# Kernel tuning notes

Measured on AMD Instinct MI355X. Metric: run time of the kernel, lower is better.

## Reference

```python
import jax, jax.numpy as jnp
import numpy as np

B_SZ, SEQ, D_MODEL = 1, 2048, 1024
D_IN, N_STATE, DT_RANK, KSIZE = 2048, 16, 64, 3


def setup_inputs() -> dict:
    key = jax.random.key(0)
    ks = jax.random.split(key, 7)
    x = jax.random.normal(ks[0], (B_SZ, SEQ, D_MODEL), jnp.float32)
    W_in = jax.random.normal(ks[1], (D_MODEL, 2 * D_IN), jnp.float32) * 0.02
    conv_w = jax.random.normal(ks[2], (D_IN, 1, KSIZE), jnp.float32) * 0.1  # OIH, depthwise
    W_x = jax.random.normal(ks[3], (D_IN, DT_RANK + 2 * N_STATE), jnp.float32) * 0.02
    W_delta = jax.random.normal(ks[4], (DT_RANK, D_IN), jnp.float32) * 0.02
    b_delta = jnp.zeros((D_IN,), jnp.float32)
    # Keras initializer: A_log[d, n] = n+1 (arange 1..N repeated over d_in rows)
    A_log = jnp.tile(jnp.arange(1, N_STATE + 1, dtype=jnp.float32)[None, :], (D_IN, 1))
    D = jnp.ones((D_IN,), jnp.float32)
    W_out = jax.random.normal(ks[5], (D_IN, D_MODEL), jnp.float32) * 0.02
    return dict(x=x, W_in=W_in, conv_w=conv_w, W_x=W_x, W_delta=W_delta,
                b_delta=b_delta, A_log=A_log, D=D, W_out=W_out)


def selective_scan(u, delta, A, Bm, Cm, D):
    # u, delta: (b,l,d); A: (d,n); Bm, Cm: (b,l,n); D: (d,)
    dA = jnp.einsum('bld,dn->bldn', delta, A)
    dB_u = jnp.einsum('bld,bld,bln->bldn', delta, u, Bm)
    # shift dA left by one step, zero at the end (matches pad+slice in source)
    dA_shift = jnp.concatenate([dA[:, 1:], jnp.zeros_like(dA[:, :1])], axis=1)
    # reversed cumulative sum along time, then exp
    dA_cs = jnp.exp(jnp.flip(jnp.cumsum(jnp.flip(dA_shift, axis=1), axis=1), axis=1))
    xs = jnp.cumsum(dB_u * dA_cs, axis=1) / (dA_cs + 1e-12)
    y = jnp.einsum('bldn,bln->bld', xs, Cm)
    return y + u * D


def reference(x, W_in, conv_w, W_x, W_delta, b_delta, A_log, D, W_out):
    d_in = conv_w.shape[0]
    ksz = conv_w.shape[2]
    n = A_log.shape[1]
    dtr = W_delta.shape[0]
    x_and_res = x @ W_in                       # (b,l,2*d_in)
    xi, res = x_and_res[..., :d_in], x_and_res[..., d_in:]
    # depthwise causal conv over time (channels_first with left padding k-1)
    xc = jnp.transpose(xi, (0, 2, 1))          # (b,d_in,l)
    xc = jax.lax.conv_general_dilated(
        xc, conv_w, window_strides=(1,), padding=[(ksz - 1, 0)],
        dimension_numbers=('NCH', 'OIH', 'NCH'), feature_group_count=d_in)
    xi = jnp.transpose(xc, (0, 2, 1))          # (b,l,d_in)
    xi = xi * jax.nn.sigmoid(xi)               # swish
    # SSM
    A = -jnp.exp(A_log)
    x_dbl = xi @ W_x                           # (b,l,dtr+2n)
    delta_lr = x_dbl[..., :dtr]
    Bm = x_dbl[..., dtr:dtr + n]
    Cm = x_dbl[..., dtr + n:]
    delta = jax.nn.softplus(delta_lr @ W_delta + b_delta)
    y = selective_scan(xi, delta, A, Bm, Cm, D)
    y = y * (res * jax.nn.sigmoid(res))
    return y @ W_out
```

## Files before the change

### kernel.cpp

```cpp
#include <hip/hip_runtime.h>
#include <hip/hip_bf16.h>
#include <math.h>

#define SEQ     2048
#define D_MODEL 1024
#define D_IN    2048
#define N_STATE 16
#define DT_RANK 64
#define XDBL_W  96
#define XDBL_LD 128
#define LC      64
#define NCH     32
#define DT      32
#define WX_KSPLIT 16
#define WX_KSEG   (D_IN / WX_KSPLIT)
#define OUT_KSPLIT 4
#define OUT_KSEG   (D_IN / OUT_KSPLIT)

#define LOG2E   1.4426950408889634f

typedef __attribute__((ext_vector_type(8))) _Float16 f16x8;
typedef __attribute__((ext_vector_type(4))) float f32x4;

__device__ __forceinline__ float fast_exp2(float x) { return __builtin_amdgcn_exp2f(x); }
__device__ __forceinline__ float fast_rcp(float x)  { return __builtin_amdgcn_rcpf(x); }

__device__ __forceinline__ ushort f2h(float x) {
    _Float16 h = (_Float16)x;
    return __builtin_bit_cast(ushort, h);
}
__device__ __forceinline__ float h2f(ushort u) {
    return (float)__builtin_bit_cast(_Float16, u);
}

__device__ __forceinline__ void gload16(const ushort* g, ushort* l) {
    __builtin_amdgcn_global_load_lds(
        (const __attribute__((address_space(1))) void*)g,
        (__attribute__((address_space(3))) void*)l, 16, 0, 0);
}

#define GL_DEFS                                                                \
    const int lane8 = lane >> 3;                                               \
    const int scol  = (lane & 7) ^ lane8;                                      \
    const int wq    = wave * 8;

#define STAGE_GL(SRC, DST, BASE, LDK, KOFF)                                    \
    _Pragma("unroll")                                                          \
    for (int q = 0; q < 4; ++q) {                                              \
        const int rr = q * 32 + wq + lane8;                                    \
        gload16(&SRC[(size_t)((BASE) + rr) * (LDK) + (KOFF) + scol * 8],       \
                ((ushort*)DST) + (q * 256 + wave * 64) * 8);                   \
    }

#define COMPUTE_KS(KS)                                                         \
    {                                                                          \
        const int slot = ((((KS) << 2) | l4) ^ sw) * 8;                        \
        f16x8 ah[4], al[4], bb[4];                                             \
        _Pragma("unroll")                                                      \
        for (int f = 0; f < 4; ++f) {                                          \
            const int ar = mw + f * 16 + l15;                                  \
            const int br = nw + f * 16 + l15;                                  \
            ah[f] = *(const f16x8*)&lA[0][ar][slot];                           \
            al[f] = *(const f16x8*)&lA[1][ar][slot];                           \
            bb[f] = *(const f16x8*)&lB[br][slot];                              \
        }                                                                      \
        _Pragma("unroll")                                                      \
        for (int i = 0; i < 4; ++i)                                            \
            _Pragma("unroll")                                                  \
            for (int j = 0; j < 4; ++j) {                                      \
                acc[i][j] = __builtin_amdgcn_mfma_f32_16x16x32_f16(            \
                    ah[i], bb[j], acc[i][j], 0, 0, 0);                         \
                acc[i][j] = __builtin_amdgcn_mfma_f32_16x16x32_f16(            \
                    al[i], bb[j], acc[i][j], 0, 0, 0);                         \
            }                                                                  \
    }

template <int CTRL>
__device__ __forceinline__ float dpp_add(float x) {
    int y = __builtin_amdgcn_update_dpp(0, __float_as_int(x), CTRL, 0xF, 0xF, true);
    return x + __int_as_float(y);
}

__global__ __launch_bounds__(256) void split_f16(
    const float* __restrict__ in, ushort* __restrict__ hi,
    ushort* __restrict__ lo)
{
    const int i = blockIdx.x * 256 + threadIdx.x;
    const float4 v = *(const float4*)&in[(size_t)i * 4];
    ushort4 h, l;
    h.x = f2h(v.x); l.x = f2h(v.x - h2f(h.x));
    h.y = f2h(v.y); l.y = f2h(v.y - h2f(h.y));
    h.z = f2h(v.z); l.z = f2h(v.z - h2f(h.z));
    h.w = f2h(v.w); l.w = f2h(v.w - h2f(h.w));
    *(ushort4*)&hi[(size_t)i * 4] = h;
    *(ushort4*)&lo[(size_t)i * 4] = l;
}

__global__ __launch_bounds__(256) void trans_f16(
    const float* __restrict__ in, ushort* __restrict__ out, int R, int C)
{
    __shared__ float tile[32][33];
    const int c0 = blockIdx.x * 32;
    const int r0 = blockIdx.y * 32;
    const int tc = threadIdx.x & 31;
    const int tr = threadIdx.x >> 5;
#pragma unroll
    for (int q = 0; q < 4; ++q)
        tile[tr + 8 * q][tc] = in[(size_t)(r0 + tr + 8 * q) * C + c0 + tc];
    __syncthreads();
#pragma unroll
    for (int q = 0; q < 4; ++q)
        out[(size_t)(c0 + tr + 8 * q) * R + r0 + tc] = f2h(tile[tc][tr + 8 * q]);
}

__global__ __launch_bounds__(256) void trans_f16_pad(
    const float* __restrict__ in, ushort* __restrict__ out, int R, int Csrc)
{
    __shared__ float tile[32][33];
    const int c0 = blockIdx.x * 32;
    const int r0 = blockIdx.y * 32;
    const int tc = threadIdx.x & 31;
    const int tr = threadIdx.x >> 5;
#pragma unroll
    for (int q = 0; q < 4; ++q) {
        const int c = c0 + tc;
        tile[tr + 8 * q][tc] =
            (c < Csrc) ? in[(size_t)(r0 + tr + 8 * q) * Csrc + c] : 0.f;
    }
    __syncthreads();
#pragma unroll
    for (int q = 0; q < 4; ++q)
        out[(size_t)(c0 + tr + 8 * q) * R + r0 + tc] = f2h(tile[tc][tr + 8 * q]);
}

__global__ __launch_bounds__(256) void gemm_mfma3(
    const ushort* __restrict__ Ahi, const ushort* __restrict__ Alo,
    const ushort* __restrict__ Bf,
    float* __restrict__ C0, float* __restrict__ C1, int nsplit,
    int M, int N, int K, int ldc0, int ldc1)
{
    __shared__ ushort lA[2][128][64];
    __shared__ ushort lB[128][64];

    const int t    = threadIdx.x;
    const int m0   = blockIdx.y * 128;
    const int n0   = blockIdx.x * 128;
    const int wave = t >> 6;
    const int lane = t & 63;
    const int mw   = (wave & 1) * 64;
    const int nw   = (wave >> 1) * 64;
    const int l15  = lane & 15;
    const int l4   = lane >> 4;
    const int sw   = l15 & 7;
    GL_DEFS

    f32x4 acc[4][4];
#pragma unroll
    for (int i = 0; i < 4; ++i)
#pragma unroll
        for (int j = 0; j < 4; ++j)
            acc[i][j] = (f32x4){0.f, 0.f, 0.f, 0.f};

    for (int k0 = 0; k0 < K; k0 += 64) {
        __syncthreads();
        STAGE_GL(Ahi, lA[0], m0, K, k0)
        STAGE_GL(Alo, lA[1], m0, K, k0)
        STAGE_GL(Bf,  lB,    n0, K, k0)
        __syncthreads();
        COMPUTE_KS(0)
        COMPUTE_KS(1)
    }

#pragma unroll
    for (int i = 0; i < 4; ++i) {
        const int rowg = m0 + mw + i * 16 + l4 * 4;
#pragma unroll
        for (int j = 0; j < 4; ++j) {
            const int colg = n0 + nw + j * 16 + l15;
            if (colg < nsplit) {
#pragma unroll
                for (int v = 0; v < 4; ++v)
                    C0[(size_t)(rowg + v) * ldc0 + colg] = acc[i][j][v];
            } else {
                const int cc = colg - nsplit;
#pragma unroll
                for (int v = 0; v < 4; ++v) {
                    const float r = acc[i][j][v];
                    C1[(size_t)(rowg + v) * ldc1 + cc] =
                        r * fast_rcp(1.f + fast_exp2(-LOG2E * r));
                }
            }
        }
    }
}

__global__ __launch_bounds__(256) void gemm_wx_mfma(
    const ushort* __restrict__ Ahi, const ushort* __restrict__ Alo,
    const ushort* __restrict__ Bf, float* __restrict__ part)
{
    __shared__ ushort lA[2][128][64];
    __shared__ ushort lB[128][64];

    const int t    = threadIdx.x;
    const int kb   = blockIdx.x;
    const int m0   = blockIdx.y * 128;
    const int wave = t >> 6;
    const int lane = t & 63;
    const int mw   = (wave & 1) * 64;
    const int nw   = (wave >> 1) * 64;
    const int l15  = lane & 15;
    const int l4   = lane >> 4;
    const int sw   = l15 & 7;
    const int kbase = kb * WX_KSEG;
    GL_DEFS

    f32x4 acc[4][4];
#pragma unroll
    for (int i = 0; i < 4; ++i)
#pragma unroll
        for (int j = 0; j < 4; ++j)
            acc[i][j] = (f32x4){0.f, 0.f, 0.f, 0.f};

    for (int k0 = 0; k0 < WX_KSEG; k0 += 64) {
        __syncthreads();
        STAGE_GL(Ahi, lA[0], m0, D_IN, kbase + k0)
        STAGE_GL(Alo, lA[1], m0, D_IN, kbase + k0)
        STAGE_GL(Bf,  lB,    0,  D_IN, kbase + k0)
        __syncthreads();
        COMPUTE_KS(0)
        COMPUTE_KS(1)
    }

#pragma unroll
    for (int i = 0; i < 4; ++i) {
        const int rowg = m0 + mw + i * 16 + l4 * 4;
#pragma unroll
        for (int j = 0; j < 4; ++j) {
            const int colg = nw + j * 16 + l15;
#pragma unroll
            for (int v = 0; v < 4; ++v)
                part[((size_t)kb * SEQ + rowg + v) * XDBL_LD + colg] =
                    acc[i][j][v];
        }
    }
}

__global__ __launch_bounds__(256) void wx_reduce(
    const float* __restrict__ part, float* __restrict__ xdbl)
{
    const size_t i = (size_t)(blockIdx.x * 256 + threadIdx.x) * 4;
    float4 s = *(const float4*)&part[i];
#pragma unroll
    for (int kb = 1; kb < WX_KSPLIT; ++kb) {
        const float4 v = *(const float4*)&part[(size_t)kb * SEQ * XDBL_LD + i];
        s.x += v.x; s.y += v.y; s.z += v.z; s.w += v.w;
    }
    *(float4*)&xdbl[i] = s;
}

__global__ __launch_bounds__(256) void gemm_out_mfma(
    const ushort* __restrict__ Ahi, const ushort* __restrict__ Alo,
    const ushort* __restrict__ Bf,
    float* __restrict__ p01, float* __restrict__ p23)
{
    __shared__ ushort lA[2][128][64];
    __shared__ ushort lB[128][64];

    const int t    = threadIdx.x;
    const int n0   = blockIdx.x * 128;
    const int m0   = blockIdx.y * 128;
    const int kb   = blockIdx.z;
    const int wave = t >> 6;
    const int lane = t & 63;
    const int mw   = (wave & 1) * 64;
    const int nw   = (wave >> 1) * 64;
    const int l15  = lane & 15;
    const int l4   = lane >> 4;
    const int sw   = l15 & 7;
    const int kbase = kb * OUT_KSEG;
    GL_DEFS

    f32x4 acc[4][4];
#pragma unroll
    for (int i = 0; i < 4; ++i)
#pragma unroll
        for (int j = 0; j < 4; ++j)
            acc[i][j] = (f32x4){0.f, 0.f, 0.f, 0.f};

    for (int k0 = 0; k0 < OUT_KSEG; k0 += 64) {
        __syncthreads();
        STAGE_GL(Ahi, lA[0], m0, D_IN, kbase + k0)
        STAGE_GL(Alo, lA[1], m0, D_IN, kbase + k0)
        STAGE_GL(Bf,  lB,    n0, D_IN, kbase + k0)
        __syncthreads();
        COMPUTE_KS(0)
        COMPUTE_KS(1)
    }

    float* base = (kb & 2) ? p23 : p01;
    base += (size_t)(kb & 1) * SEQ * D_MODEL;
#pragma unroll
    for (int i = 0; i < 4; ++i) {
        const int rowg = m0 + mw + i * 16 + l4 * 4;
#pragma unroll
        for (int j = 0; j < 4; ++j) {
            const int colg = n0 + nw + j * 16 + l15;
#pragma unroll
            for (int v = 0; v < 4; ++v)
                base[(size_t)(rowg + v) * D_MODEL + colg] = acc[i][j][v];
        }
    }
}

__global__ __launch_bounds__(256) void out_reduce(
    const float* __restrict__ p01, const float* __restrict__ p23,
    float* __restrict__ out)
{
    const size_t i = (size_t)(blockIdx.x * 256 + threadIdx.x) * 4;
    const size_t MN = (size_t)SEQ * D_MODEL;
    const float4 a = *(const float4*)&p01[i];
    const float4 b = *(const float4*)&p01[i + MN];
    const float4 c = *(const float4*)&p23[i];
    const float4 d = *(const float4*)&p23[i + MN];
    float4 s;
    s.x = ((a.x + b.x) + c.x) + d.x;
    s.y = ((a.y + b.y) + c.y) + d.y;
    s.z = ((a.z + b.z) + c.z) + d.z;
    s.w = ((a.w + b.w) + c.w) + d.w;
    *(float4*)&out[i] = s;
}

__global__ __launch_bounds__(256) void gemm128(
    const float* __restrict__ A, const float* __restrict__ B,
    float* __restrict__ C, int M, int N, int K,
    int lda, int ldb, int ldc,
    const float* __restrict__ bias, int act)
{
    __shared__ float As[16][132];
    __shared__ float Bs[16][132];

    const int t   = threadIdx.x;
    const int bn0 = blockIdx.x * 128;
    const int bm0 = blockIdx.y * 128;
    const int tx  = t & 15;
    const int ty  = t >> 4;

    const int ar  = t >> 2;
    const int ak  = (t & 3) * 4;
    const int bk  = t >> 5;
    const int bn4 = (t & 31) * 4;

    float acc[8][8];
#pragma unroll
    for (int i = 0; i < 8; ++i)
#pragma unroll
        for (int j = 0; j < 8; ++j) acc[i][j] = 0.f;

    for (int k0 = 0; k0 < K; k0 += 16) {
        float4 a0 = *(const float4*)&A[(size_t)(bm0 + ar)      * lda + k0 + ak];
        float4 a1 = *(const float4*)&A[(size_t)(bm0 + ar + 64) * lda + k0 + ak];
        float4 b0 = *(const float4*)&B[(size_t)(k0 + bk)     * ldb + bn0 + bn4];
        float4 b1 = *(const float4*)&B[(size_t)(k0 + bk + 8) * ldb + bn0 + bn4];

        __syncthreads();
        As[ak + 0][ar] = a0.x; As[ak + 1][ar] = a0.y;
        As[ak + 2][ar] = a0.z; As[ak + 3][ar] = a0.w;
        As[ak + 0][ar + 64] = a1.x; As[ak + 1][ar + 64] = a1.y;
        As[ak + 2][ar + 64] = a1.z; As[ak + 3][ar + 64] = a1.w;
        *(float4*)&Bs[bk][bn4]     = b0;
        *(float4*)&Bs[bk + 8][bn4] = b1;
        __syncthreads();

#pragma unroll
        for (int kk = 0; kk < 16; ++kk) {
            float a[8], b[8];
            ((float4*)a)[0] = *(const float4*)&As[kk][ty * 8];
            ((float4*)a)[1] = *(const float4*)&As[kk][ty * 8 + 4];
            ((float4*)b)[0] = *(const float4*)&Bs[kk][tx * 8];
            ((float4*)b)[1] = *(const float4*)&Bs[kk][tx * 8 + 4];
#pragma unroll
            for (int i = 0; i < 8; ++i)
#pragma unroll
                for (int j = 0; j < 8; ++j)
                    acc[i][j] = fmaf(a[i], b[j], acc[i][j]);
        }
    }

    const int row = bm0 + ty * 8;
    const int col = bn0 + tx * 8;
#pragma unroll
    for (int i = 0; i < 8; ++i) {
        float vals[8];
#pragma unroll
        for (int j = 0; j < 8; ++j) {
            float v = acc[i][j];
            if (act == 1) {
                v += bias[col + j];
                v = (v > 20.f) ? v : log1pf(__expf(v));
            }
            vals[j] = v;
        }
        *(float4*)&C[(size_t)(row + i) * ldc + col]     = ((float4*)vals)[0];
        *(float4*)&C[(size_t)(row + i) * ldc + col + 4] = ((float4*)vals)[1];
    }
}

__global__ __launch_bounds__(256) void conv_silu_split(
    const float* __restrict__ xi, const float* __restrict__ cw,
    float* __restrict__ u, ushort* __restrict__ uhi, ushort* __restrict__ ulo)
{
    const int id = blockIdx.x * 256 + threadIdx.x;
    const int l = id >> 11;
    const int d = id & (D_IN - 1);
    const float w0 = cw[d * 3 + 0];
    const float w1 = cw[d * 3 + 1];
    const float w2 = cw[d * 3 + 2];
    const float x0  = xi[(size_t)l * D_IN + d];
    const float xm1 = (l >= 1) ? xi[(size_t)(l - 1) * D_IN + d] : 0.f;
    const float xm2 = (l >= 2) ? xi[(size_t)(l - 2) * D_IN + d] : 0.f;
    const float v = w0 * xm2 + w1 * xm1 + w2 * x0;
    const float s = fast_rcp(1.f + fast_exp2(-LOG2E * v));
    const float uu = v * s;
    u[id] = uu;
    const ushort h = f2h(uu);
    uhi[id] = h;
    ulo[id] = f2h(uu - h2f(h));
}

__global__ __launch_bounds__(256) void csum64(
    const float* __restrict__ delta, double* __restrict__ csum)
{
    const int d = blockIdx.x * 256 + threadIdx.x;
    const int c = blockIdx.y;
    double s = 0.0;
    for (int i = 0; i < LC; ++i)
        s += (double)delta[(size_t)(c * LC + i) * D_IN + d];
    csum[(size_t)c * D_IN + d] = s;
}

__global__ __launch_bounds__(256) void chunk_prefix(
    const double* __restrict__ csum, double* __restrict__ P0,
    double* __restrict__ Td)
{
    const int d = blockIdx.x * 256 + threadIdx.x;
    double P = 0.0;
    for (int c = 0; c < NCH; ++c) {
        P0[(size_t)c * D_IN + d] = P;
        P += csum[(size_t)c * D_IN + d];
    }
    Td[d] = P;
}

__global__ __launch_bounds__(256) void sfx_precompute(
    const float* __restrict__ delta, const double* __restrict__ P0,
    const double* __restrict__ Td, float* __restrict__ sfx)
{
    const int d = blockIdx.x * 256 + threadIdx.x;
    const int c = blockIdx.y;
    double P = P0[(size_t)c * D_IN + d];
    const double T = Td[d];
    for (int i = 0; i < LC; ++i) {
        const size_t row = (size_t)(c * LC + i) * D_IN + d;
        P += (double)delta[row];
        sfx[row] = (float)fmax(T - P, 0.0);
    }
}

__global__ __launch_bounds__(512) void scan_partA(
    const float* __restrict__ delta, const float* __restrict__ u,
    const float* __restrict__ sfxbuf, const float* __restrict__ xdbl,
    const float* __restrict__ Alog, float* __restrict__ Wc)
{
    __shared__ float2 spA[LC][DT];
    __shared__ float  sBA[LC][16];

    const int t  = threadIdx.x;
    const int c  = blockIdx.x;
    const int d0 = blockIdx.y * DT;

    {
        const int r = t >> 3, c4 = (t & 7) * 4;
        const size_t row = (size_t)(c * LC + r) * D_IN + d0 + c4;
        const float4 dv4 = *(const float4*)&delta[row];
        const float4 uv4 = *(const float4*)&u[row];
        const float4 sx4 = *(const float4*)&sfxbuf[row];
        spA[r][c4 + 0] = make_float2(dv4.x * uv4.x, sx4.x);
        spA[r][c4 + 1] = make_float2(dv4.y * uv4.y, sx4.y);
        spA[r][c4 + 2] = make_float2(dv4.z * uv4.z, sx4.z);
        spA[r][c4 + 3] = make_float2(dv4.w * uv4.w, sx4.w);
    }
    if (t < 256) {
        const int r = t >> 2, c4 = (t & 3) * 4;
        *(float4*)&sBA[r][c4] =
            *(const float4*)&xdbl[(size_t)(c * LC + r) * XDBL_LD + DT_RANK + c4];
    }
    __syncthreads();

    const int n  = t & 15;
    const int dq = t >> 4;
    const int d  = d0 + dq;
    const float An2 = -expf(Alog[d * N_STATE + n]) * LOG2E;

    float W = 0.f;
#pragma unroll
    for (int i = 0; i < LC; ++i) {
        const float2 p = spA[i][dq];
        W = fmaf(p.x * sBA[i][n], fast_exp2(An2 * p.y), W);
    }
    Wc[((size_t)c * D_IN + d) * N_STATE + n] = W;
}

__global__ __launch_bounds__(256) void scan_combine(float* __restrict__ Wc)
{
    const int id = blockIdx.x * 256 + threadIdx.x;
    float W = 0.f;
    for (int c = 0; c < NCH; ++c) {
        const size_t idx = (size_t)c * (D_IN * N_STATE) + id;
        const float w = Wc[idx];
        Wc[idx] = W;
        W += w;
    }
}

__global__ __launch_bounds__(512) void scan_partC(
    const float* __restrict__ delta, const float* __restrict__ u,
    const float* __restrict__ xdbl, const float* __restrict__ W0buf,
    const float* __restrict__ sfxbuf, const float* __restrict__ Alog,
    const float* __restrict__ Dvec, const float* __restrict__ rgbuf,
    float* __restrict__ yg)
{
    __shared__ float4 spack[LC][DT];
    __shared__ float2 sbc[LC][16];

    const int t  = threadIdx.x;
    const int c  = blockIdx.x;
    const int d0 = blockIdx.y * DT;

    {
        const int r = t >> 3, c4 = (t & 7) * 4;
        const size_t row = (size_t)(c * LC + r) * D_IN + d0 + c4;
        const float4 dv4 = *(const float4*)&delta[row];
        const float4 uv4 = *(const float4*)&u[row];
        const float4 sx4 = *(const float4*)&sfxbuf[row];
        const float4 rg4 = *(const float4*)&rgbuf[row];
        spack[r][c4 + 0] = make_float4(dv4.x * uv4.x, sx4.x, uv4.x, rg4.x);
        spack[r][c4 + 1] = make_float4(dv4.y * uv4.y, sx4.y, uv4.y, rg4.y);
        spack[r][c4 + 2] = make_float4(dv4.z * uv4.z, sx4.z, uv4.z, rg4.z);
        spack[r][c4 + 3] = make_float4(dv4.w * uv4.w, sx4.w, uv4.w, rg4.w);
    }
    if (t < 256) {
        const int r = t >> 2, n4 = (t & 3) * 4;
        const float4 b4 = *(const float4*)&xdbl[(size_t)(c * LC + r) * XDBL_LD + DT_RANK + n4];
        const float4 c4v = *(const float4*)&xdbl[(size_t)(c * LC + r) * XDBL_LD + DT_RANK + 16 + n4];
        sbc[r][n4 + 0] = make_float2(b4.x, c4v.x);
        sbc[r][n4 + 1] = make_float2(b4.y, c4v.y);
        sbc[r][n4 + 2] = make_float2(b4.z, c4v.z);
        sbc[r][n4 + 3] = make_float2(b4.w, c4v.w);
    }
    __syncthreads();

    const int n  = t & 15;
    const int dq = t >> 4;
    const int d  = d0 + dq;
    const float An2 = -expf(Alog[d * N_STATE + n]) * LOG2E;
    const float Dd = Dvec[d];

    float W = W0buf[((size_t)c * D_IN + d) * N_STATE + n];

#pragma unroll
    for (int i = 0; i < LC; ++i) {
        const float4 p = spack[i][dq];
        const float2 bc = sbc[i][n];
        const float E = fast_exp2(An2 * p.y);
        W = fmaf(p.x * bc.x, E, W);
        const float xs = W * fast_rcp(E + 1e-12f);
        float contrib = xs * bc.y;
        contrib = dpp_add<0xB1>(contrib);
        contrib = dpp_add<0x4E>(contrib);
        contrib = dpp_add<0x128>(contrib);
        contrib = dpp_add<0x124>(contrib);
        if (n == 0) {
            yg[(size_t)(c * LC + i) * D_IN + d] =
                fmaf(p.z, Dd, contrib) * p.w;
        }
    }
}

extern "C" void kernel_launch(void* const* d_in, const int* in_sizes, int n_in,
                              void* d_out, int out_size, void* d_ws, size_t ws_size,
                              hipStream_t stream)
{
    const float* x      = (const float*)d_in[0];
    const float* W_in   = (const float*)d_in[1];
    const float* conv_w = (const float*)d_in[2];
    const float* W_x    = (const float*)d_in[3];
    const float* W_del  = (const float*)d_in[4];
    const float* b_del  = (const float*)d_in[5];
    const float* A_log  = (const float*)d_in[6];
    const float* Dv     = (const float*)d_in[7];
    const float* W_out  = (const float*)d_in[8];
    float* out = (float*)d_out;

    char* ws = (char*)d_ws;
    float*  xi    = (float*)(ws + 0);
    float*  wxp   = (float*)(ws + 0);
    float*  sfx   = (float*)(ws + 0);
    ushort* yg_hi = (ushort*)(ws + 0);
    ushort* yg_lo = (ushort*)(ws + 8388608);
    float*  rg    = (float*)(ws + 16777216);
    float*  p01   = (float*)(ws + 16777216);
    ushort* x_hi  = (ushort*)(ws + 33554432);
    ushort* x_lo  = (ushort*)(ws + 37748736);
    float*  u     = (float*)(ws + 33554432);
    ushort* wo    = (ushort*)(ws + 33554432);
    float*  xdbl  = (float*)(ws + 50331648);
    ushort* wi    = (ushort*)(ws + 51380224);
    ushort* u_hi  = (ushort*)(ws + 51380224);
    ushort* u_lo  = (ushort*)(ws + 59768832);
    float*  delta = (float*)(ws + 51380224);
    float*  p23   = (float*)(ws + 51380224);
    float*  Wc    = (float*)(ws + 68157440);
    double* csum  = (double*)(ws + 72351744);
    double* P0    = (double*)(ws + 72876032);
    double* Td    = (double*)(ws + 73400320);
    ushort* wx    = (ushort*)(ws + 73416704);
    float*  yg    = delta;

    trans_f16<<<dim3(4096 / 32, 1024 / 32), 256, 0, stream>>>(
        W_in, wi, 1024, 4096);

    split_f16<<<(SEQ * D_MODEL / 4) / 256, 256, 0, stream>>>(x, x_hi, x_lo);

    gemm_mfma3<<<dim3(4096 / 128, 2048 / 128), 256, 0, stream>>>(
        x_hi, x_lo, wi, xi, rg, D_IN,
        SEQ, 2 * D_IN, D_MODEL, D_IN, D_IN);

    conv_silu_split<<<(SEQ * D_IN) / 256, 256, 0, stream>>>(
        xi, conv_w, u, u_hi, u_lo);

    trans_f16_pad<<<dim3(XDBL_LD / 32, D_IN / 32), 256, 0, stream>>>(
        W_x, wx, D_IN, XDBL_W);

    gemm_wx_mfma<<<dim3(WX_KSPLIT, SEQ / 128), 256, 0, stream>>>(
        u_hi, u_lo, wx, wxp);
    wx_reduce<<<(SEQ * XDBL_LD / 4) / 256, 256, 0, stream>>>(wxp, xdbl);

    gemm128<<<dim3(2048 / 128, 2048 / 128), 256, 0, stream>>>(
        xdbl, W_del, delta, SEQ, D_IN, DT_RANK, XDBL_LD, D_IN, D_IN,
        b_del, 1);

    csum64<<<dim3(D_IN / 256, NCH), 256, 0, stream>>>(delta, csum);
    chunk_prefix<<<D_IN / 256, 256, 0, stream>>>(csum, P0, Td);
    sfx_precompute<<<dim3(D_IN / 256, NCH), 256, 0, stream>>>(delta, P0, Td, sfx);

    scan_partA<<<dim3(NCH, D_IN / DT), 512, 0, stream>>>(
        delta, u, sfx, xdbl, A_log, Wc);
    scan_combine<<<(D_IN * N_STATE) / 256, 256, 0, stream>>>(Wc);
    scan_partC<<<dim3(NCH, D_IN / DT), 512, 0, stream>>>(
        delta, u, xdbl, Wc, sfx, A_log, Dv, rg, yg);

    split_f16<<<(SEQ * D_IN / 4) / 256, 256, 0, stream>>>(yg, yg_hi, yg_lo);

    trans_f16<<<dim3(1024 / 32, 2048 / 32), 256, 0, stream>>>(
        W_out, wo, 2048, 1024);

    gemm_out_mfma<<<dim3(D_MODEL / 128, SEQ / 128, OUT_KSPLIT), 256, 0, stream>>>(
        yg_hi, yg_lo, wo, p01, p23);
    out_reduce<<<(SEQ * D_MODEL / 4) / 256, 256, 0, stream>>>(p01, p23, out);
}
```

Before: 240.0 us.

## Fuse chunk delta sums into delta GEMM epilogue and halve scan threads

The softplus delta GEMM epilogue now computes per-64-row chunk column sums in double and writes them directly. This removes the separate csum64 and chunk_prefix kernels, and sfx_precompute derives its prefix and total from csum itself. The scan partA and partC kernels now use 256 threads, each handling two state indices, which halves block size and shortens the DPP reduction. The cost is extra double-precision work and shared memory in the GEMM epilogue, redundant prefix loops in every sfx block, and scalar rather than float4 loads in the scan kernels.

```diff
diff --git a/kernel.cpp b/kernel.cpp
--- a/kernel.cpp
+++ b/kernel.cpp
@@ -334,10 +334,11 @@
     const float* __restrict__ A, const float* __restrict__ B,
     float* __restrict__ C, int M, int N, int K,
     int lda, int ldb, int ldc,
-    const float* __restrict__ bias, int act)
+    const float* __restrict__ bias, double* __restrict__ csumOut)
 {
     __shared__ float As[16][132];
     __shared__ float Bs[16][132];
+    __shared__ double dpart[16][128];
 
     const int t   = threadIdx.x;
     const int bn0 = blockIdx.x * 128;
@@ -388,20 +389,33 @@
 
     const int row = bm0 + ty * 8;
     const int col = bn0 + tx * 8;
+    double dsum[8];
+#pragma unroll
+    for (int j = 0; j < 8; ++j) dsum[j] = 0.0;
 #pragma unroll
     for (int i = 0; i < 8; ++i) {
         float vals[8];
 #pragma unroll
         for (int j = 0; j < 8; ++j) {
-            float v = acc[i][j];
-            if (act == 1) {
-                v += bias[col + j];
-                v = (v > 20.f) ? v : log1pf(__expf(v));
-            }
+            float v = acc[i][j] + bias[col + j];
+            v = (v > 20.f) ? v : log1pf(__expf(v));
             vals[j] = v;
+            dsum[j] += (double)v;
         }
         *(float4*)&C[(size_t)(row + i) * ldc + col]     = ((float4*)vals)[0];
         *(float4*)&C[(size_t)(row + i) * ldc + col + 4] = ((float4*)vals)[1];
+    }
+
+#pragma unroll
+    for (int j = 0; j < 8; ++j) dpart[ty][tx * 8 + j] = dsum[j];
+    __syncthreads();
+    {
+        const int colr = t & 127;
+        const int half = t >> 7;
+        double s = 0.0;
+#pragma unroll
+        for (int q = 0; q < 8; ++q) s += dpart[half * 8 + q][colr];
+        csumOut[(size_t)((bm0 >> 6) + half) * D_IN + bn0 + colr] = s;
     }
 }
 
@@ -427,38 +441,18 @@
     ulo[id] = f2h(uu - h2f(h));
 }
 
-__global__ __launch_bounds__(256) void csum64(
-    const float* __restrict__ delta, double* __restrict__ csum)
+__global__ __launch_bounds__(256) void sfx_precompute(
+    const float* __restrict__ delta, const double* __restrict__ csum,
+    float* __restrict__ sfx)
 {
     const int d = blockIdx.x * 256 + threadIdx.x;
     const int c = blockIdx.y;
-    double s = 0.0;
-    for (int i = 0; i < LC; ++i)
-        s += (double)delta[(size_t)(c * LC + i) * D_IN + d];
-    csum[(size_t)c * D_IN + d] = s;
-}
-
-__global__ __launch_bounds__(256) void chunk_prefix(
-    const double* __restrict__ csum, double* __restrict__ P0,
-    double* __restrict__ Td)
-{
-    const int d = blockIdx.x * 256 + threadIdx.x;
-    double P = 0.0;
-    for (int c = 0; c < NCH; ++c) {
-        P0[(size_t)c * D_IN + d] = P;
-        P += csum[(size_t)c * D_IN + d];
-    }
-    Td[d] = P;
-}
-
-__global__ __launch_bounds__(256) void sfx_precompute(
-    const float* __restrict__ delta, const double* __restrict__ P0,
-    const double* __restrict__ Td, float* __restrict__ sfx)
-{
-    const int d = blockIdx.x * 256 + threadIdx.x;
-    const int c = blockIdx.y;
-    double P = P0[(size_t)c * D_IN + d];
-    const double T = Td[d];
+    double S = 0.0, P = 0.0;
+    for (int c2 = 0; c2 < NCH; ++c2) {
+        if (c2 == c) P = S;
+        S += csum[(size_t)c2 * D_IN + d];
+    }
+    const double T = S;
     for (int i = 0; i < LC; ++i) {
         const size_t row = (size_t)(c * LC + i) * D_IN + d;
         P += (double)delta[row];
@@ -466,48 +460,51 @@
     }
 }
 
-__global__ __launch_bounds__(512) void scan_partA(
+__global__ __launch_bounds__(256) void scan_partA(
     const float* __restrict__ delta, const float* __restrict__ u,
     const float* __restrict__ sfxbuf, const float* __restrict__ xdbl,
     const float* __restrict__ Alog, float* __restrict__ Wc)
 {
     __shared__ float2 spA[LC][DT];
-    __shared__ float  sBA[LC][16];
+    __shared__ float2 sbA[LC][8];
 
     const int t  = threadIdx.x;
     const int c  = blockIdx.x;
     const int d0 = blockIdx.y * DT;
 
-    {
-        const int r = t >> 3, c4 = (t & 7) * 4;
-        const size_t row = (size_t)(c * LC + r) * D_IN + d0 + c4;
-        const float4 dv4 = *(const float4*)&delta[row];
-        const float4 uv4 = *(const float4*)&u[row];
-        const float4 sx4 = *(const float4*)&sfxbuf[row];
-        spA[r][c4 + 0] = make_float2(dv4.x * uv4.x, sx4.x);
-        spA[r][c4 + 1] = make_float2(dv4.y * uv4.y, sx4.y);
-        spA[r][c4 + 2] = make_float2(dv4.z * uv4.z, sx4.z);
-        spA[r][c4 + 3] = make_float2(dv4.w * uv4.w, sx4.w);
-    }
-    if (t < 256) {
-        const int r = t >> 2, c4 = (t & 3) * 4;
-        *(float4*)&sBA[r][c4] =
-            *(const float4*)&xdbl[(size_t)(c * LC + r) * XDBL_LD + DT_RANK + c4];
+#pragma unroll
+    for (int q = 0; q < 8; ++q) {
+        const int e = q * 256 + t;
+        const int r = e >> 5, col = e & 31;
+        const size_t row = (size_t)(c * LC + r) * D_IN + d0 + col;
+        spA[r][col] = make_float2(delta[row] * u[row], sfxbuf[row]);
+    }
+#pragma unroll
+    for (int q = 0; q < 2; ++q) {
+        const int e = q * 256 + t;
+        const int r = e >> 3, n8e = e & 7;
+        const size_t base = (size_t)(c * LC + r) * XDBL_LD + DT_RANK;
+        sbA[r][n8e] = make_float2(xdbl[base + n8e], xdbl[base + 8 + n8e]);
     }
     __syncthreads();
 
-    const int n  = t & 15;
-    const int dq = t >> 4;
+    const int dq = t >> 3;
+    const int n8 = t & 7;
     const int d  = d0 + dq;
-    const float An2 = -expf(Alog[d * N_STATE + n]) * LOG2E;
-
-    float W = 0.f;
+    const float An2a = -expf(Alog[d * N_STATE + n8]) * LOG2E;
+    const float An2b = -expf(Alog[d * N_STATE + n8 + 8]) * LOG2E;
+
+    float W0 = 0.f, W1 = 0.f;
 #pragma unroll
     for (int i = 0; i < LC; ++i) {
         const float2 p = spA[i][dq];
-        W = fmaf(p.x * sBA[i][n], fast_exp2(An2 * p.y), W);
-    }
-    Wc[((size_t)c * D_IN + d) * N_STATE + n] = W;
+        const float2 b = sbA[i][n8];
+        W0 = fmaf(p.x * b.x, fast_exp2(An2a * p.y), W0);
+        W1 = fmaf(p.x * b.y, fast_exp2(An2b * p.y), W1);
+    }
+    const size_t o = ((size_t)c * D_IN + d) * N_STATE + n8;
+    Wc[o]     = W0;
+    Wc[o + 8] = W1;
 }
 
 __global__ __launch_bounds__(256) void scan_combine(float* __restrict__ Wc)
@@ -522,7 +519,7 @@
     }
 }
 
-__global__ __launch_bounds__(512) void scan_partC(
+__global__ __launch_bounds__(256) void scan_partC(
     const float* __restrict__ delta, const float* __restrict__ u,
     const float* __restrict__ xdbl, const float* __restrict__ W0buf,
     const float* __restrict__ sfxbuf, const float* __restrict__ Alog,
@@ -530,56 +527,57 @@
     float* __restrict__ yg)
 {
     __shared__ float4 spack[LC][DT];
-    __shared__ float2 sbc[LC][16];
+    __shared__ float4 sbc[LC][8];
 
     const int t  = threadIdx.x;
     const int c  = blockIdx.x;
     const int d0 = blockIdx.y * DT;
 
-    {
-        const int r = t >> 3, c4 = (t & 7) * 4;
-        const size_t row = (size_t)(c * LC + r) * D_IN + d0 + c4;
-        const float4 dv4 = *(const float4*)&delta[row];
-        const float4 uv4 = *(const float4*)&u[row];
-        const float4 sx4 = *(const float4*)&sfxbuf[row];
-        const float4 rg4 = *(const float4*)&rgbuf[row];
-        spack[r][c4 + 0] = make_float4(dv4.x * uv4.x, sx4.x, uv4.x, rg4.x);
-        spack[r][c4 + 1] = make_float4(dv4.y * uv4.y, sx4.y, uv4.y, rg4.y);
-        spack[r][c4 + 2] = make_float4(dv4.z * uv4.z, sx4.z, uv4.z, rg4.z);
-        spack[r][c4 + 3] = make_float4(dv4.w * uv4.w, sx4.w, uv4.w, rg4.w);
-    }
-    if (t < 256) {
-        const int r = t >> 2, n4 = (t & 3) * 4;
-        const float4 b4 = *(const float4*)&xdbl[(size_t)(c * LC + r) * XDBL_LD + DT_RANK + n4];
-        const float4 c4v = *(const float4*)&xdbl[(size_t)(c * LC + r) * XDBL_LD + DT_RANK + 16 + n4];
-        sbc[r][n4 + 0] = make_float2(b4.x, c4v.x);
-        sbc[r][n4 + 1] = make_float2(b4.y, c4v.y);
-        sbc[r][n4 + 2] = make_float2(b4.z, c4v.z);
-        sbc[r][n4 + 3] = make_float2(b4.w, c4v.w);
+#pragma unroll
+    for (int q = 0; q < 8; ++q) {
+        const int e = q * 256 + t;
+        const int r = e >> 5, col = e & 31;
+        const size_t row = (size_t)(c * LC + r) * D_IN + d0 + col;
+        const float dv = delta[row];
+        const float uv = u[row];
+        spack[r][col] = make_float4(dv * uv, sfxbuf[row], uv, rgbuf[row]);
+    }
+#pragma unroll
+    for (int q = 0; q < 2; ++q) {
+        const int e = q * 256 + t;
+        const int r = e >> 3, n8e = e & 7;
+        const size_t base = (size_t)(c * LC + r) * XDBL_LD + DT_RANK;
+        sbc[r][n8e] = make_float4(xdbl[base + n8e],      xdbl[base + 16 + n8e],
+                                  xdbl[base + 8 + n8e],  xdbl[base + 24 + n8e]);
     }
     __syncthreads();
 
-    const int n  = t & 15;
-    const int dq = t >> 4;
+    const int dq = t >> 3;
+    const int n8 = t & 7;
     const int d  = d0 + dq;
-    const float An2 = -expf(Alog[d * N_STATE + n]) * LOG2E;
+    const float An2a = -expf(Alog[d * N_STATE + n8]) * LOG2E;
+    const float An2b = -expf(Alog[d * N_STATE + n8 + 8]) * LOG2E;
     const float Dd = Dvec[d];
 
-    float W = W0buf[((size_t)c * D_IN + d) * N_STATE + n];
+    const size_t wo = ((size_t)c * D_IN + d) * N_STATE + n8;
+    float W0 = W0buf[wo];
+    float W1 = W0buf[wo + 8];
 
 #pragma unroll
     for (int i = 0; i < LC; ++i) {
-        const float4 p = spack[i][dq];
-        const float2 bc = sbc[i][n];
-        const float E = fast_exp2(An2 * p.y);
-        W = fmaf(p.x * bc.x, E, W);
-        const float xs = W * fast_rcp(E + 1e-12f);
-        float contrib = xs * bc.y;
+        const float4 p  = spack[i][dq];
+        const float4 bc = sbc[i][n8];
+        const float E0 = fast_exp2(An2a * p.y);
+        const float E1 = fast_exp2(An2b * p.y);
+        W0 = fmaf(p.x * bc.x, E0, W0);
+        W1 = fmaf(p.x * bc.z, E1, W1);
+        const float xs0 = W0 * fast_rcp(E0 + 1e-12f);
+        const float xs1 = W1 * fast_rcp(E1 + 1e-12f);
+        float contrib = fmaf(xs0, bc.y, xs1 * bc.w);
         contrib = dpp_add<0xB1>(contrib);
         contrib = dpp_add<0x4E>(contrib);
-        contrib = dpp_add<0x128>(contrib);
         contrib = dpp_add<0x124>(contrib);
-        if (n == 0) {
+        if (n8 == 0) {
             yg[(size_t)(c * LC + i) * D_IN + d] =
                 fmaf(p.z, Dd, contrib) * p.w;
         }
@@ -621,8 +619,6 @@
     float*  p23   = (float*)(ws + 51380224);
     float*  Wc    = (float*)(ws + 68157440);
     double* csum  = (double*)(ws + 72351744);
-    double* P0    = (double*)(ws + 72876032);
-    double* Td    = (double*)(ws + 73400320);
     ushort* wx    = (ushort*)(ws + 73416704);
     float*  yg    = delta;
 
@@ -647,16 +643,14 @@
 
     gemm128<<<dim3(2048 / 128, 2048 / 128), 256, 0, stream>>>(
         xdbl, W_del, delta, SEQ, D_IN, DT_RANK, XDBL_LD, D_IN, D_IN,
-        b_del, 1);
-
-    csum64<<<dim3(D_IN / 256, NCH), 256, 0, stream>>>(delta, csum);
-    chunk_prefix<<<D_IN / 256, 256, 0, stream>>>(csum, P0, Td);
-    sfx_precompute<<<dim3(D_IN / 256, NCH), 256, 0, stream>>>(delta, P0, Td, sfx);
-
-    scan_partA<<<dim3(NCH, D_IN / DT), 512, 0, stream>>>(
+        b_del, csum);
+
+    sfx_precompute<<<dim3(D_IN / 256, NCH), 256, 0, stream>>>(delta, csum, sfx);
+
+    scan_partA<<<dim3(NCH, D_IN / DT), 256, 0, stream>>>(
         delta, u, sfx, xdbl, A_log, Wc);
     scan_combine<<<(D_IN * N_STATE) / 256, 256, 0, stream>>>(Wc);
-    scan_partC<<<dim3(NCH, D_IN / DT), 512, 0, stream>>>(
+    scan_partC<<<dim3(NCH, D_IN / DT), 256, 0, stream>>>(
         delta, u, xdbl, Wc, sfx, A_log, Dv, rg, yg);
 
     split_f16<<<(SEQ * D_IN / 4) / 256, 256, 0, stream>>>(yg, yg_hi, yg_lo);
```

Result: faster. 225.9 us (-5.9%).
